# Kernel tuning notes

Measured on AMD Instinct MI355X. Metric: run time of the kernel, lower is better.

## Reference

```python
import jax, jax.numpy as jnp
import numpy as np
import itertools, string

# Weight space: 2-layer MLP params, flattened in dict-key order (W1, W2, b1, b2).
SPECS = [(0, 1), (1, 2), (1,), (2,)]
N = 1024            # size of each permutable dim (perm ids 0,1,2)
C_IN, C_OUT = 16, 16
NUM_TERMS = [9, 10, 7, 6]   # equivariant basis terms per output leaf


def _set_partitions(elems):
    if not elems:
        yield []
        return
    first, rest = elems[0], elems[1:]
    for part in _set_partitions(rest):
        for i in range(len(part)):
            yield part[:i] + [part[i] + [first]] + part[i + 1:]
        yield part + [[first]]


def gen_basis(out_spec, in_spec, out_dims, x):
    """All permutation-equivariant basis maps from x (*in_dims, c) to (*out_dims, c).
    Basis elements <-> set partitions of (in,out) axis positions sharing a perm id:
    in-axes in a block are diagonalized; in-only blocks are summed; mixed blocks copy
    the axis to the matching out position; out-only blocks broadcast."""
    pos = ([('in', a, p) for a, p in enumerate(in_spec)]
           + [('out', a, p) for a, p in enumerate(out_spec)])
    by_pid = {}
    for q in pos:
        by_pid.setdefault(q[2], []).append(q)
    parts = [list(_set_partitions(by_pid[p])) for p in sorted(by_pid)]
    terms = []
    for combo in itertools.product(*parts):
        blocks = [b for part in combo for b in part]
        pos2b = {(q[0], q[1]): bi for bi, b in enumerate(blocks) for q in b}
        L = string.ascii_lowercase
        in_sub = ''.join(L[pos2b[('in', a)]] for a in range(len(in_spec)))
        mixed = [bi for bi, b in enumerate(blocks)
                 if any(q[0] == 'in' for q in b) and any(q[0] == 'out' for q in b)]
        out_sub = ''.join(L[bi] for bi in mixed)
        # diagonal over repeated in-axes, sum over in-only blocks; z = channel axis
        t = jnp.einsum(f'{in_sub}z->{out_sub}z', x)
        targets = [min(q[1] for q in blocks[bi] if q[0] == 'out') for bi in mixed]
        t = jnp.transpose(t, list(np.argsort(targets)) + [len(mixed)])
        st = sorted(targets)
        for ax in range(len(out_dims)):
            if ax not in st:
                t = jnp.expand_dims(t, ax)
        t = jnp.broadcast_to(t, tuple(out_dims) + (x.shape[-1],))
        for b in blocks:  # diagonal-embed blocks with >1 out axis (not hit for MLP specs)
            outs = sorted(q[1] for q in b if q[0] == 'out')
            for a1, a2 in zip(outs, outs[1:]):
                n = out_dims[a1]
                sh = [1] * (len(out_dims) + 1)
                sh[a1] = n; sh[a2] = n
                t = t * jnp.eye(n, dtype=x.dtype).reshape(sh)
        terms.append(t)
    return terms


def _forward(flat, thetas, biases):
    outs = []
    for i in range(len(flat)):
        out_dims = flat[i].shape[:-1]
        acc = jnp.zeros(tuple(out_dims) + (C_OUT,), dtype=flat[i].dtype)
        k = 0
        for j in range(len(flat)):
            for term in gen_basis(SPECS[i], SPECS[j], out_dims, flat[j]):
                acc = acc + jnp.einsum('...i,io->...o', term, thetas[i][k])
                k += 1
        outs.append(acc + biases[i])
    return tuple(outs)


def setup_inputs() -> dict:
    key = jax.random.key(0)
    ks = jax.random.split(key, 12)
    inp = {
        'W1': jax.random.normal(ks[0], (N, N, C_IN), jnp.float32),
        'W2': jax.random.normal(ks[1], (N, N, C_IN), jnp.float32),
        'b1': jax.random.normal(ks[2], (N, C_IN), jnp.float32),
        'b2': jax.random.normal(ks[3], (N, C_IN), jnp.float32),
    }
    for i, k in enumerate(NUM_TERMS):
        scale = (1.0 / (C_IN * k)) ** 0.5
        inp[f'theta_{i}'] = scale * jax.random.normal(ks[4 + i], (k, C_IN, C_OUT), jnp.float32)
        inp[f'bias_{i}'] = jnp.zeros((C_OUT,), jnp.float32)
    return inp


def reference(W1, W2, b1, b2, theta_0, theta_1, theta_2, theta_3,
              bias_0, bias_1, bias_2, bias_3):
    return _forward([W1, W2, b1, b2],
                    [theta_0, theta_1, theta_2, theta_3],
                    [bias_0, bias_1, bias_2, bias_3])
```

## Files before the change

### kernel.cpp

```cpp
#include <hip/hip_runtime.h>

#define NDIM 1024
#define CH 16
#define ROW_F4 4096

__device__ inline float4 f4add(float4 a, float4 b) {
    return make_float4(a.x + b.x, a.y + b.y, a.z + b.z, a.w + b.w);
}
__device__ inline float4 f4zero() { return make_float4(0.f, 0.f, 0.f, 0.f); }

__global__ __launch_bounds__(256) void k_fused(const float* __restrict__ W1,
                                               const float* __restrict__ W2,
                                               float* __restrict__ rowpart,
                                               float* __restrict__ colpart,
                                               float* __restrict__ tiletot) {
    int t  = threadIdx.x;
    int jt = blockIdx.x, it = blockIdx.y, z = blockIdx.z;
    const float4* base = (const float4*)(z ? W2 : W1)
                       + (size_t)it * 32 * ROW_F4 + jt * 256 + t;
    __shared__ float4 tile[8][258];
    __shared__ float4 rtotL[32];
    float4 colacc = f4zero();
    float4 rtot   = f4zero();
    for (int s = 0; s < 4; ++s) {
        if (s) __syncthreads();
#pragma unroll
        for (int r = 0; r < 8; ++r) {
            float4 v = base[(size_t)(s * 8 + r) * ROW_F4];
            colacc = f4add(colacc, v);
            tile[r][t] = v;
        }
        __syncthreads();
        if (t < 32) {
            int r = t >> 2, cq = t & 3;
            float4 sv = f4zero();
#pragma unroll
            for (int jl = 0; jl < 64; ++jl) sv = f4add(sv, tile[r][jl * 4 + cq]);
            ((float4*)rowpart)[(size_t)(z * 16 + jt) * 4096
                               + (it * 32 + s * 8 + r) * 4 + cq] = sv;
            rtot = f4add(rtot, sv);
        }
    }
    ((float4*)colpart)[(size_t)(z * 32 + it) * 4096 + jt * 256 + t] = colacc;
    if (t < 32) rtotL[t] = rtot;
    __syncthreads();
    if (t < 4) {
        float4 sv = f4zero();
#pragma unroll
        for (int r = 0; r < 8; ++r) sv = f4add(sv, rtotL[r * 4 + t]);
        ((float4*)tiletot)[(size_t)(z * 512 + it * 16 + jt) * 4 + t] = sv;
    }
}

__global__ __launch_bounds__(256) void k_mid(const float* __restrict__ rowpart,
                                             const float* __restrict__ colpart,
                                             const float* __restrict__ tiletot,
                                             const float* __restrict__ b1,
                                             const float* __restrict__ b2,
                                             const float* __restrict__ th0,
                                             const float* __restrict__ th1,
                                             const float* __restrict__ th2,
                                             const float* __restrict__ th3,
                                             const float* __restrict__ bias0,
                                             const float* __restrict__ bias1,
                                             const float* __restrict__ bias2,
                                             const float* __restrict__ bias3,
                                             float* __restrict__ R0, float* __restrict__ C0,
                                             float* __restrict__ R1, float* __restrict__ C1,
                                             float* __restrict__ out2, float* __restrict__ out3) {
    int t  = threadIdx.x;
    int i0 = blockIdx.x * 16;
    __shared__ float sums[64];
    __shared__ float ldsA[2][8][16], ldsB[2][8][16];
    __shared__ float Ars1[16][16], Ars2[16][16], Acs1[16][16], Acs2[16][16];

    {
        int z = t >> 7, c = t & 15, p = (t >> 4) & 7;
        float s = 0.f;
#pragma unroll 8
        for (int m = 0; m < 64; ++m)
            s += tiletot[(size_t)(z * 512 + p * 64 + m) * 16 + c];
        ldsA[z][p][c] = s;
        const float* bb = z ? b2 : b1;
        s = 0.f;
#pragma unroll 8
        for (int m = 0; m < 128; ++m)
            s += bb[(size_t)(p * 128 + m) * 16 + c];
        ldsB[z][p][c] = s;
    }
    int il = t >> 4, o = t & 15, i = i0 + il;
    {
        float s1 = 0.f, s2 = 0.f, s3 = 0.f, s4 = 0.f;
#pragma unroll 4
        for (int k = 0; k < 16; ++k) {
            s1 += rowpart[(size_t)k * 16384 + i * 16 + o];
            s2 += rowpart[(size_t)(16 + k) * 16384 + i * 16 + o];
        }
#pragma unroll 8
        for (int k = 0; k < 32; ++k) {
            s3 += colpart[(size_t)k * 16384 + i * 16 + o];
            s4 += colpart[(size_t)(32 + k) * 16384 + i * 16 + o];
        }
        Ars1[il][o] = s1; Ars2[il][o] = s2; Acs1[il][o] = s3; Acs2[il][o] = s4;
    }
    __syncthreads();
    if (t < 32) {
        int z = t >> 4, cc = t & 15;
        float r = 0.f;
#pragma unroll
        for (int q = 0; q < 8; ++q) r += ldsA[z][q][cc];
        sums[z * 16 + cc] = r;
    } else if (t < 64) {
        int z = (t - 32) >> 4, cc = t & 15;
        float r = 0.f;
#pragma unroll
        for (int q = 0; q < 8; ++q) r += ldsB[z][q][cc];
        sums[32 + z * 16 + cc] = r;
    }
    __syncthreads();

    const float* b1i = b1 + i * 16;
    const float* b2i = b2 + i * 16;
    float r0 = 0.f, c0a = 0.f, r1 = 0.f, c1a = 0.f, o2 = 0.f, o3 = 0.f;
    float k0 = 0.f, k1 = 0.f, k2 = 0.f, k3 = 0.f;
#pragma unroll
    for (int c = 0; c < 16; ++c) {
        float sW1 = sums[c], sW2 = sums[16 + c], sb1 = sums[32 + c], sb2 = sums[48 + c];
        float rs1 = Ars1[il][c], rs2 = Ars2[il][c];
        float cs1 = Acs1[il][c], cs2 = Acs2[il][c];
        float vb1 = b1i[c], vb2 = b2i[c];
        r0  += rs1 * th0[(1 * 16 + c) * 16 + o];
        c0a += cs1 * th0[(2 * 16 + c) * 16 + o]
             + rs2 * th0[(4 * 16 + c) * 16 + o]
             + vb1 * th0[(6 * 16 + c) * 16 + o];
        k0  += sW1 * th0[(3 * 16 + c) * 16 + o] + sW2 * th0[(5 * 16 + c) * 16 + o]
             + sb1 * th0[(7 * 16 + c) * 16 + o] + sb2 * th0[(8 * 16 + c) * 16 + o];
        r1  += cs1 * th1[(0 * 16 + c) * 16 + o]
             + rs2 * th1[(3 * 16 + c) * 16 + o]
             + vb1 * th1[(6 * 16 + c) * 16 + o];
        c1a += cs2 * th1[(4 * 16 + c) * 16 + o]
             + vb2 * th1[(8 * 16 + c) * 16 + o];
        k1  += sW1 * th1[(1 * 16 + c) * 16 + o] + sW2 * th1[(5 * 16 + c) * 16 + o]
             + sb1 * th1[(7 * 16 + c) * 16 + o] + sb2 * th1[(9 * 16 + c) * 16 + o];
        o2  += cs1 * th2[(0 * 16 + c) * 16 + o]
             + rs2 * th2[(2 * 16 + c) * 16 + o]
             + vb1 * th2[(4 * 16 + c) * 16 + o];
        k2  += sW1 * th2[(1 * 16 + c) * 16 + o] + sW2 * th2[(3 * 16 + c) * 16 + o]
             + sb1 * th2[(5 * 16 + c) * 16 + o] + sb2 * th2[(6 * 16 + c) * 16 + o];
        o3  += cs2 * th3[(1 * 16 + c) * 16 + o]
             + vb2 * th3[(4 * 16 + c) * 16 + o];
        k3  += sW1 * th3[(0 * 16 + c) * 16 + o] + sW2 * th3[(2 * 16 + c) * 16 + o]
             + sb1 * th3[(3 * 16 + c) * 16 + o] + sb2 * th3[(5 * 16 + c) * 16 + o];
    }
    int gt = i * 16 + o;
    R0[gt]   = r0;
    C0[gt]   = c0a + k0 + bias0[o];
    R1[gt]   = r1;
    C1[gt]   = c1a + k1 + bias1[o];
    out2[gt] = o2 + k2 + bias2[o];
    out3[gt] = o3 + k3 + bias3[o];
}

__global__ __launch_bounds__(256) void k_main(const float* __restrict__ W1,
                                              const float* __restrict__ W2,
                                              const float* __restrict__ R0,
                                              const float* __restrict__ C0,
                                              const float* __restrict__ R1,
                                              const float* __restrict__ C1,
                                              const float* __restrict__ th0,
                                              const float* __restrict__ th1,
                                              float* __restrict__ out0,
                                              float* __restrict__ out1) {
    int z = blockIdx.z;
    const float* __restrict__ W  = z ? W2 : W1;
    const float* __restrict__ R  = z ? R1 : R0;
    const float* __restrict__ Cc = z ? C1 : C0;
    const float* __restrict__ TH = z ? th1 : th0;
    float* __restrict__ out      = z ? out1 : out0;

    int t  = threadIdx.x;
    int i  = blockIdx.y;
    int jb = blockIdx.x * 256;

    __shared__ float4 xs[1280];

    const float4* Wf4 = (const float4*)W + (size_t)i * 4096 + jb * 4;
    float4*       Of4 = (float4*)out    + (size_t)i * 4096 + jb * 4;

#pragma unroll
    for (int q = 0; q < 4; ++q) {
        int g = t + 256 * q;
        xs[5 * (g >> 2) + (g & 3)] = Wf4[g];
    }
    __syncthreads();

    float x[16];
#pragma unroll
    for (int k = 0; k < 4; ++k) {
        float4 v = xs[5 * t + k];
        x[4 * k] = v.x; x[4 * k + 1] = v.y; x[4 * k + 2] = v.z; x[4 * k + 3] = v.w;
    }
    const float4* cj = (const float4*)(Cc + (size_t)(jb + t) * 16);
    float4 c0 = cj[0], c1 = cj[1], c2 = cj[2], c3 = cj[3];
    float acc[16] = {c0.x, c0.y, c0.z, c0.w, c1.x, c1.y, c1.z, c1.w,
                     c2.x, c2.y, c2.z, c2.w, c3.x, c3.y, c3.z, c3.w};
#pragma unroll
    for (int o = 0; o < 16; ++o) acc[o] += R[i * 16 + o];
#pragma unroll
    for (int c = 0; c < 16; ++c) {
        float xv = x[c];
#pragma unroll
        for (int o = 0; o < 16; ++o) acc[o] += xv * TH[c * 16 + o];
    }
    __syncthreads();
#pragma unroll
    for (int k = 0; k < 4; ++k)
        xs[5 * t + k] = make_float4(acc[4 * k], acc[4 * k + 1],
                                    acc[4 * k + 2], acc[4 * k + 3]);
    __syncthreads();
#pragma unroll
    for (int q = 0; q < 4; ++q) {
        int g = t + 256 * q;
        Of4[g] = xs[5 * (g >> 2) + (g & 3)];
    }
}

extern "C" void kernel_launch(void* const* d_in, const int* in_sizes, int n_in,
                              void* d_out, int out_size, void* d_ws, size_t ws_size,
                              hipStream_t stream) {
    const float* W1    = (const float*)d_in[0];
    const float* W2    = (const float*)d_in[1];
    const float* b1    = (const float*)d_in[2];
    const float* b2    = (const float*)d_in[3];
    const float* th0   = (const float*)d_in[4];
    const float* bias0 = (const float*)d_in[5];
    const float* th1   = (const float*)d_in[6];
    const float* bias1 = (const float*)d_in[7];
    const float* th2   = (const float*)d_in[8];
    const float* bias2 = (const float*)d_in[9];
    const float* th3   = (const float*)d_in[10];
    const float* bias3 = (const float*)d_in[11];

    float* out  = (float*)d_out;
    float* out0 = out;
    float* out1 = out + (size_t)NDIM * NDIM * CH;
    float* out2 = out1 + (size_t)NDIM * NDIM * CH;
    float* out3 = out2 + (size_t)NDIM * CH;

    float* rowpart = out0;
    float* colpart = out0 + 524288;
    float* tiletot = out0 + 1572864;

    float* ws = (float*)d_ws;
    float* R0 = ws;
    float* C0 = R0 + 16384;
    float* R1 = C0 + 16384;
    float* C1 = R1 + 16384;

    k_fused<<<dim3(16, 32, 2), dim3(256), 0, stream>>>(W1, W2, rowpart, colpart, tiletot);
    k_mid<<<dim3(64), dim3(256), 0, stream>>>(rowpart, colpart, tiletot, b1, b2,
                                              th0, th1, th2, th3,
                                              bias0, bias1, bias2, bias3,
                                              R0, C0, R1, C1, out2, out3);
    k_main<<<dim3(4, NDIM, 2), dim3(256), 0, stream>>>(W1, W2, R0, C0, R1, C1,
                                                       th0, th1 + 2 * 256,
                                                       out0, out1);
}
```

Before: 99.26 us.

## Shrink reduction tiles to 8 rows and process two column tiles per main block

The first reduction kernel now has each block handle 8 rows instead of 32, giving four times as many blocks. This raises parallelism but produces four times as many column partials, which the mid kernel must then sum. The main kernel now processes 512 columns per block instead of 256, and it stages theta and the row term in shared memory so they are reused across two independent accumulator sets. The cost is more partial-sum traffic through the output scratch and higher register and LDS use per block in the main kernel.

Result: slower. 115.4 us (+16.3%).

```diff
diff --git a/kernel.cpp b/kernel.cpp
--- a/kernel.cpp
+++ b/kernel.cpp
@@ -17,38 +17,32 @@
     int t  = threadIdx.x;
     int jt = blockIdx.x, it = blockIdx.y, z = blockIdx.z;
     const float4* base = (const float4*)(z ? W2 : W1)
-                       + (size_t)it * 32 * ROW_F4 + jt * 256 + t;
+                       + (size_t)it * 8 * ROW_F4 + jt * 256 + t;
     __shared__ float4 tile[8][258];
-    __shared__ float4 rtotL[32];
+    __shared__ float4 rtot[32];
     float4 colacc = f4zero();
-    float4 rtot   = f4zero();
-    for (int s = 0; s < 4; ++s) {
-        if (s) __syncthreads();
-#pragma unroll
-        for (int r = 0; r < 8; ++r) {
-            float4 v = base[(size_t)(s * 8 + r) * ROW_F4];
-            colacc = f4add(colacc, v);
-            tile[r][t] = v;
-        }
-        __syncthreads();
-        if (t < 32) {
-            int r = t >> 2, cq = t & 3;
-            float4 sv = f4zero();
-#pragma unroll
-            for (int jl = 0; jl < 64; ++jl) sv = f4add(sv, tile[r][jl * 4 + cq]);
-            ((float4*)rowpart)[(size_t)(z * 16 + jt) * 4096
-                               + (it * 32 + s * 8 + r) * 4 + cq] = sv;
-            rtot = f4add(rtot, sv);
-        }
-    }
-    ((float4*)colpart)[(size_t)(z * 32 + it) * 4096 + jt * 256 + t] = colacc;
-    if (t < 32) rtotL[t] = rtot;
+#pragma unroll
+    for (int r = 0; r < 8; ++r) {
+        float4 v = base[(size_t)r * ROW_F4];
+        colacc = f4add(colacc, v);
+        tile[r][t] = v;
+    }
+    ((float4*)colpart)[(size_t)(z * 128 + it) * 4096 + jt * 256 + t] = colacc;
+    __syncthreads();
+    if (t < 32) {
+        int r = t >> 2, cq = t & 3;
+        float4 s = f4zero();
+#pragma unroll
+        for (int jl = 0; jl < 64; ++jl) s = f4add(s, tile[r][jl * 4 + cq]);
+        ((float4*)rowpart)[(size_t)(z * 16 + jt) * 4096 + (it * 8 + r) * 4 + cq] = s;
+        rtot[t] = s;
+    }
     __syncthreads();
     if (t < 4) {
-        float4 sv = f4zero();
-#pragma unroll
-        for (int r = 0; r < 8; ++r) sv = f4add(sv, rtotL[r * 4 + t]);
-        ((float4*)tiletot)[(size_t)(z * 512 + it * 16 + jt) * 4 + t] = sv;
+        float4 s = f4zero();
+#pragma unroll
+        for (int r = 0; r < 8; ++r) s = f4add(s, rtot[r * 4 + t]);
+        ((float4*)tiletot)[(size_t)(z * 2048 + it * 16 + jt) * 4 + t] = s;
     }
 }
 
@@ -78,8 +72,8 @@
         int z = t >> 7, c = t & 15, p = (t >> 4) & 7;
         float s = 0.f;
 #pragma unroll 8
-        for (int m = 0; m < 64; ++m)
-            s += tiletot[(size_t)(z * 512 + p * 64 + m) * 16 + c];
+        for (int m = 0; m < 256; ++m)
+            s += tiletot[(size_t)(z * 2048 + p * 256 + m) * 16 + c];
         ldsA[z][p][c] = s;
         const float* bb = z ? b2 : b1;
         s = 0.f;
@@ -97,9 +91,9 @@
             s2 += rowpart[(size_t)(16 + k) * 16384 + i * 16 + o];
         }
 #pragma unroll 8
-        for (int k = 0; k < 32; ++k) {
+        for (int k = 0; k < 128; ++k) {
             s3 += colpart[(size_t)k * 16384 + i * 16 + o];
-            s4 += colpart[(size_t)(32 + k) * 16384 + i * 16 + o];
+            s4 += colpart[(size_t)(128 + k) * 16384 + i * 16 + o];
         }
         Ars1[il][o] = s1; Ars2[il][o] = s2; Acs1[il][o] = s3; Acs2[il][o] = s4;
     }
@@ -180,48 +174,71 @@
 
     int t  = threadIdx.x;
     int i  = blockIdx.y;
-    int jb = blockIdx.x * 256;
-
-    __shared__ float4 xs[1280];
+    int jb = blockIdx.x * 512;
+
+    __shared__ float4 xsA[1280];
+    __shared__ float4 xsB[1280];
+    __shared__ float  th[256];
+    __shared__ float  r[16];
 
     const float4* Wf4 = (const float4*)W + (size_t)i * 4096 + jb * 4;
     float4*       Of4 = (float4*)out    + (size_t)i * 4096 + jb * 4;
 
+    th[t] = TH[t];
+    if (t < 16) r[t] = R[i * 16 + t];
 #pragma unroll
     for (int q = 0; q < 4; ++q) {
         int g = t + 256 * q;
-        xs[5 * (g >> 2) + (g & 3)] = Wf4[g];
-    }
-    __syncthreads();
-
-    float x[16];
+        xsA[5 * (g >> 2) + (g & 3)] = Wf4[g];
+        xsB[5 * (g >> 2) + (g & 3)] = Wf4[1024 + g];
+    }
+    __syncthreads();
+
+    float xA[16], xB[16];
 #pragma unroll
     for (int k = 0; k < 4; ++k) {
-        float4 v = xs[5 * t + k];
-        x[4 * k] = v.x; x[4 * k + 1] = v.y; x[4 * k + 2] = v.z; x[4 * k + 3] = v.w;
-    }
-    const float4* cj = (const float4*)(Cc + (size_t)(jb + t) * 16);
-    float4 c0 = cj[0], c1 = cj[1], c2 = cj[2], c3 = cj[3];
-    float acc[16] = {c0.x, c0.y, c0.z, c0.w, c1.x, c1.y, c1.z, c1.w,
-                     c2.x, c2.y, c2.z, c2.w, c3.x, c3.y, c3.z, c3.w};
-#pragma unroll
-    for (int o = 0; o < 16; ++o) acc[o] += R[i * 16 + o];
+        float4 va = xsA[5 * t + k];
+        float4 vb = xsB[5 * t + k];
+        xA[4 * k] = va.x; xA[4 * k + 1] = va.y; xA[4 * k + 2] = va.z; xA[4 * k + 3] = va.w;
+        xB[4 * k] = vb.x; xB[4 * k + 1] = vb.y; xB[4 * k + 2] = vb.z; xB[4 * k + 3] = vb.w;
+    }
+    const float4* cjA = (const float4*)(Cc + (size_t)(jb + t) * 16);
+    const float4* cjB = (const float4*)(Cc + (size_t)(jb + 256 + t) * 16);
+    float accA[16], accB[16];
+#pragma unroll
+    for (int q = 0; q < 4; ++q) {
+        float4 ca = cjA[q], cb = cjB[q];
+        accA[q * 4 + 0] = ca.x + r[q * 4 + 0]; accB[q * 4 + 0] = cb.x + r[q * 4 + 0];
+        accA[q * 4 + 1] = ca.y + r[q * 4 + 1]; accB[q * 4 + 1] = cb.y + r[q * 4 + 1];
+        accA[q * 4 + 2] = ca.z + r[q * 4 + 2]; accB[q * 4 + 2] = cb.z + r[q * 4 + 2];
+        accA[q * 4 + 3] = ca.w + r[q * 4 + 3]; accB[q * 4 + 3] = cb.w + r[q * 4 + 3];
+    }
 #pragma unroll
     for (int c = 0; c < 16; ++c) {
-        float xv = x[c];
-#pragma unroll
-        for (int o = 0; o < 16; ++o) acc[o] += xv * TH[c * 16 + o];
-    }
-    __syncthreads();
-#pragma unroll
-    for (int k = 0; k < 4; ++k)
-        xs[5 * t + k] = make_float4(acc[4 * k], acc[4 * k + 1],
-                                    acc[4 * k + 2], acc[4 * k + 3]);
+        float tv[16];
+#pragma unroll
+        for (int o = 0; o < 16; ++o) tv[o] = th[c * 16 + o];
+        float xa = xA[c], xb = xB[c];
+#pragma unroll
+        for (int o = 0; o < 16; ++o) {
+            accA[o] += xa * tv[o];
+            accB[o] += xb * tv[o];
+        }
+    }
+    __syncthreads();
+#pragma unroll
+    for (int k = 0; k < 4; ++k) {
+        xsA[5 * t + k] = make_float4(accA[4 * k], accA[4 * k + 1],
+                                     accA[4 * k + 2], accA[4 * k + 3]);
+        xsB[5 * t + k] = make_float4(accB[4 * k], accB[4 * k + 1],
+                                     accB[4 * k + 2], accB[4 * k + 3]);
+    }
     __syncthreads();
 #pragma unroll
     for (int q = 0; q < 4; ++q) {
         int g = t + 256 * q;
-        Of4[g] = xs[5 * (g >> 2) + (g & 3)];
+        Of4[g]        = xsA[5 * (g >> 2) + (g & 3)];
+        Of4[1024 + g] = xsB[5 * (g >> 2) + (g & 3)];
     }
 }
 
@@ -249,7 +266,7 @@
 
     float* rowpart = out0;
     float* colpart = out0 + 524288;
-    float* tiletot = out0 + 1572864;
+    float* tiletot = out0 + 4718592;
 
     float* ws = (float*)d_ws;
     float* R0 = ws;
@@ -257,12 +274,12 @@
     float* R1 = C0 + 16384;
     float* C1 = R1 + 16384;
 
-    k_fused<<<dim3(16, 32, 2), dim3(256), 0, stream>>>(W1, W2, rowpart, colpart, tiletot);
+    k_fused<<<dim3(16, 128, 2), dim3(256), 0, stream>>>(W1, W2, rowpart, colpart, tiletot);
     k_mid<<<dim3(64), dim3(256), 0, stream>>>(rowpart, colpart, tiletot, b1, b2,
                                               th0, th1, th2, th3,
                                               bias0, bias1, bias2, bias3,
                                               R0, C0, R1, C1, out2, out3);
-    k_main<<<dim3(4, NDIM, 2), dim3(256), 0, stream>>>(W1, W2, R0, C0, R1, C1,
+    k_main<<<dim3(2, NDIM, 2), dim3(256), 0, stream>>>(W1, W2, R0, C0, R1, C1,
                                                        th0, th1 + 2 * 256,
                                                        out0, out1);
 }
```
